# Optimization experiments

Measured on AMD Instinct MI355X. Metric: run time of the kernel, lower is better.

The kernel has to match this reference:

```python
import jax, jax.numpy as jnp
import numpy as np

N, G, H1, H2, HEADS, EMB, C, S = 4096, 2048, 512, 128, 8, 16, 20, 4
CH = H1 // HEADS  # per-head channels = 64
EPS = 1e-6
COEF_FE = 0.1


def _uni(k, shape, fan_in, fan_out):
    c = np.sqrt(6.0 / (fan_in + fan_out)).astype(np.float32)
    return jax.random.uniform(k, shape, jnp.float32, -c, c)


def setup_inputs() -> dict:
    key = jax.random.key(0)
    ks = jax.random.split(key, 40)
    adj = (jax.random.uniform(ks[0], (N, N)) < 0.005).astype(jnp.float32)
    adj = jnp.maximum(adj, jnp.eye(N, dtype=jnp.float32))  # self-loops, no empty rows
    node_feats = jax.random.normal(ks[1], (N, G), jnp.float32)
    count_matrix = jax.random.randint(ks[2], (N, G), 0, 50).astype(jnp.float32)
    library_size = jax.random.uniform(ks[3], (N, 1), jnp.float32, 0.5, 2.0)
    slice_label = jax.random.randint(ks[4], (N,), 0, S)
    basis = jax.random.uniform(ks[5], (C, G), jnp.float32)
    # encoder GAT layer1: HEADS heads, c_in=G -> c_out=CH each
    We1 = _uni(ks[6], (HEADS, CH, G), G, CH)
    be1 = jnp.zeros((HEADS, CH), jnp.float32)
    v0e1 = _uni(ks[7], (HEADS, CH, 1), CH, 1)
    v1e1 = _uni(ks[8], (HEADS, CH, 1), CH, 1)
    # encoder dense layer2: H1 -> H2
    W2 = _uni(ks[9], (H2, H1), H1, H2)
    b2 = jnp.zeros((H2,), jnp.float32)
    # decoder GAT layer1: c_in = H2+EMB -> CH per head
    CIN_D = H2 + EMB
    Wd1 = _uni(ks[10], (HEADS, CH, CIN_D), CIN_D, CH)
    bd1 = jnp.zeros((HEADS, CH), jnp.float32)
    v0d1 = _uni(ks[11], (HEADS, CH, 1), CH, 1)
    v1d1 = _uni(ks[12], (HEADS, CH, 1), CH, 1)
    # decoder dense layer2: H1 -> G
    Wd2 = _uni(ks[13], (G, H1), H1, G)
    bd2 = jnp.zeros((G,), jnp.float32)
    # deconv alpha (H2+EMB -> 1) and beta (H2 -> C); zero-init in torch, small random here
    Wa = 0.01 * jax.random.normal(ks[14], (1, CIN_D), jnp.float32)
    ba = jnp.zeros((1,), jnp.float32)
    Wb = 0.01 * jax.random.normal(ks[15], (C, H2), jnp.float32)
    bb = jnp.zeros((C,), jnp.float32)
    gamma = 0.01 * jax.random.normal(ks[16], (S, G), jnp.float32)
    logtheta = 5.0 * jnp.ones((S, G), jnp.float32)
    emb_table = jax.random.normal(ks[17], (S, EMB), jnp.float32)
    return dict(adj_matrix=adj, node_feats=node_feats, count_matrix=count_matrix,
                library_size=library_size, slice_label=slice_label, basis=basis,
                We1=We1, be1=be1, v0e1=v0e1, v1e1=v1e1, W2=W2, b2=b2,
                Wd1=Wd1, bd1=bd1, v0d1=v0d1, v1d1=v1d1, Wd2=Wd2, bd2=bd2,
                Wa=Wa, ba=ba, Wb=Wb, bb=bb, gamma=gamma, logtheta=logtheta,
                emb_table=emb_table)


def _gat_head(x, adj, W, b, v0, v1):
    h = x @ W.T + b                       # [N, CH]
    logits = adj * ((h @ v0) + (h @ v1).T)  # [N, N]; zero where adj==0
    s = jax.nn.sigmoid(logits) - 0.5       # unnormalized attentions
    mask = adj != 0.0
    e = jnp.where(mask, jnp.exp(s), 0.0)    # sparse softmax over structural nonzeros (temp=1)
    den = e.sum(axis=1, keepdims=True)
    p = e / jnp.where(den == 0.0, 1.0, den)
    return p @ h                            # [N, CH]


def _gat_multi(x, adj, Ws, bs, v0s, v1s):
    return jnp.concatenate([_gat_head(x, adj, Ws[i], bs[i], v0s[i], v1s[i])
                            for i in range(HEADS)], axis=1)


def reference(adj_matrix, node_feats, count_matrix, library_size, slice_label, basis,
              We1, be1, v0e1, v1e1, W2, b2, Wd1, bd1, v0d1, v1d1, Wd2, bd2,
              Wa, ba, Wb, bb, gamma, logtheta, emb_table):
    # encoder
    H = jax.nn.elu(_gat_multi(node_feats, adj_matrix, We1, be1, v0e1, v1e1))
    Z = H @ W2.T + b2                                   # [N, H2]
    emb = emb_table[slice_label]                        # [N, EMB]
    # deconvolutioner
    beta = jax.nn.softmax(jax.nn.elu(Z) @ Wb.T + bb, axis=1)   # [N, C]
    Hc = jax.nn.elu(jnp.concatenate([Z, emb], axis=1))
    alpha = Hc @ Wa.T + ba                              # [N, 1]
    # decoder
    Hd = jax.nn.elu(_gat_multi(jnp.concatenate([Z, emb], axis=1), adj_matrix,
                               Wd1, bd1, v0d1, v1d1))
    X_recon = Hd @ Wd2.T + bd2                          # [N, G]
    features_loss = jnp.mean(jnp.sqrt(jnp.sum((node_feats - X_recon) ** 2, axis=1)))
    # NB deconvolution loss
    log_lam = jnp.log(beta @ basis + EPS) + alpha + gamma[slice_label]
    lam = jnp.exp(log_lam)
    th = jnp.exp(logtheta)[slice_label]                 # [N, G]
    mu = library_size * lam
    ll = (jax.lax.lgamma(count_matrix + th + EPS) - jax.lax.lgamma(th + EPS)
          + th * jnp.log(th + EPS) - th * jnp.log(th + mu + EPS)
          + count_matrix * jnp.log(mu + EPS) - count_matrix * jnp.log(th + mu + EPS))
    decon_loss = -jnp.mean(jnp.sum(ll, axis=1))
    return decon_loss + COEF_FE * features_loss
```

## Files before the change

### kernel.cpp

```cpp
#include <hip/hip_runtime.h>
#include <hip/hip_bf16.h>
#include <math.h>

#define N 4096
#define G 2048
#define H1 512
#define H2 128
#define HEADS 8
#define EMB 16
#define C 20
#define S 4
#define CH 64
#define CIN_D (H2 + EMB)
#define KD_PAD 160
#define KB_PAD 32
#define CAP 128
#define EPSV 1e-6f

typedef __attribute__((ext_vector_type(8))) short short8;
typedef __attribute__((ext_vector_type(8))) short bf16x8;
typedef __attribute__((ext_vector_type(4))) float f32x4;

__device__ __forceinline__ unsigned short f2b(float x) {
    __hip_bfloat16 h = __float2bfloat16(x);
    return *reinterpret_cast<unsigned short*>(&h);
}
__device__ __forceinline__ float b2f(unsigned short u) {
    unsigned int x = ((unsigned int)u) << 16;
    return __uint_as_float(x);
}
__device__ __forceinline__ float lgamma_fast(float x) {
    float sh = 0.f;
    while (x < 8.f) { sh -= __logf(x); x += 1.f; }
    float ix = 1.f / x;
    float lx = __logf(x);
    return (x - 0.5f) * lx - x + 0.91893853f
         + ix * (0.08333333f - 0.00277778f * ix * ix) + sh;
}

__global__ void build_csr(const float* __restrict__ adj, int* __restrict__ col_idx,
                          int* __restrict__ row_cnt) {
    int i = blockIdx.x;
    int lane = threadIdx.x;
    int cnt = 0;
    const float4* row4 = (const float4*)(adj + (size_t)i * N);
    int* cols = col_idx + (size_t)i * CAP;
    unsigned long long lmask = (1ull << lane) - 1ull;
    for (int c = 0; c < N / 256; ++c) {
        float4 v = row4[c * 64 + lane];
        float vv[4] = {v.x, v.y, v.z, v.w};
        #pragma unroll
        for (int s = 0; s < 4; ++s) {
            unsigned long long m = __ballot(vv[s] != 0.f);
            if (vv[s] != 0.f) {
                int idx = cnt + __popcll(m & lmask);
                if (idx < CAP) cols[idx] = c * 256 + lane * 4 + s;
            }
            cnt += __popcll(m);
        }
    }
    if (lane == 0) row_cnt[i] = cnt < CAP ? cnt : CAP;
}

#define SEG_SG   (S * G)
#define SEG_NF4  (N * G / 4)
#define SEG_WE4  (H1 * G / 4)
#define SEG_W24  (H2 * H1 / 4)
#define SEG_WD1E (H1 * KD_PAD)
#define SEG_WD24 (G * H1 / 4)
#define SEG_BTE  (G * KB_PAD)
#define PREP_TOTAL (SEG_SG + SEG_NF4 + SEG_WE4 + SEG_W24 + SEG_WD1E + SEG_WD24 + SEG_BTE)

__device__ __forceinline__ void cvt4(const float* __restrict__ in,
                                     unsigned short* __restrict__ out, int i) {
    float4 v = ((const float4*)in)[i];
    ushort4 o;
    o.x = f2b(v.x); o.y = f2b(v.y); o.z = f2b(v.z); o.w = f2b(v.w);
    ((ushort4*)out)[i] = o;
}

__global__ __launch_bounds__(256) void prep(const float* __restrict__ logtheta,
                                            const float* __restrict__ gamma,
                                            float* __restrict__ th_a, float* __restrict__ eg_a,
                                            float* __restrict__ gm_a, float* __restrict__ ax_a,
                                            const float* __restrict__ node_f,
                                            unsigned short* __restrict__ nf_bf,
                                            const float* __restrict__ We1,
                                            unsigned short* __restrict__ We1_bf,
                                            const float* __restrict__ W2,
                                            unsigned short* __restrict__ W2_bf,
                                            const float* __restrict__ Wd1,
                                            unsigned short* __restrict__ Wd1_bf,
                                            const float* __restrict__ Wd2,
                                            unsigned short* __restrict__ Wd2_bf,
                                            const float* __restrict__ basis,
                                            unsigned short* __restrict__ basisT_bf) {
    int idx = blockIdx.x * 256 + threadIdx.x;
    if (idx < SEG_SG) {
        float th = __expf(logtheta[idx]);
        float gm = gamma[idx];
        th_a[idx] = th;
        eg_a[idx] = __expf(gm);
        gm_a[idx] = gm;
        ax_a[idx] = th * __logf(th + EPSV) - lgammaf(th + EPSV);
        return;
    }
    idx -= SEG_SG;
    if (idx < SEG_NF4) { cvt4(node_f, nf_bf, idx); return; }
    idx -= SEG_NF4;
    if (idx < SEG_WE4) { cvt4(We1, We1_bf, idx); return; }
    idx -= SEG_WE4;
    if (idx < SEG_W24) { cvt4(W2, W2_bf, idx); return; }
    idx -= SEG_W24;
    if (idx < SEG_WD1E) {
        int n = idx / KD_PAD, k = idx - n * KD_PAD;
        Wd1_bf[idx] = f2b(k < CIN_D ? Wd1[n * CIN_D + k] : 0.f);
        return;
    }
    idx -= SEG_WD1E;
    if (idx < SEG_WD24) { cvt4(Wd2, Wd2_bf, idx); return; }
    idx -= SEG_WD24;
    if (idx < SEG_BTE) {
        int g = idx >> 5, c = idx & 31;
        basisT_bf[idx] = f2b(c < C ? basis[c * G + g] : 0.f);
    }
}

#define LDP 40
template<int FM, int OBF, int KS>
__global__ __launch_bounds__(256) void gemm_mfma(const unsigned short* __restrict__ A,
                                                 const unsigned short* __restrict__ B,
                                                 const float* __restrict__ bias,
                                                 void* __restrict__ Cout,
                                                 int M, int Nc, int K) {
    constexpr int BMT = FM * 32;
    __shared__ short As[BMT * LDP];
    __shared__ short Bs[128 * LDP];
    int bn = blockIdx.x, bm = blockIdx.y;
    int kz = (KS > 1) ? blockIdx.z : 0;
    int t = threadIdx.x;
    int lane = t & 63, wid = t >> 6;
    int wr = wid >> 1, wc = wid & 1;
    f32x4 acc[FM][4] = {};
    const short* Ag = (const short*)A + (size_t)(bm * BMT) * K;
    const short* Bg = (const short*)B + (size_t)(bn * 128) * K;
    int r0 = t >> 2, q0 = t & 3;
    int rbase = (lane & 15);
    int koff = (lane >> 4) * 8;
    int kbeg = kz * (K / KS), kend = kbeg + K / KS;

    for (int k0 = kbeg; k0 < kend; k0 += 32) {
        short8 a0 = *(const short8*)(Ag + (size_t)r0 * K + k0 + q0 * 8);
        short8 a1;
        if constexpr (FM == 4) a1 = *(const short8*)(Ag + (size_t)(r0 + 64) * K + k0 + q0 * 8);
        short8 b0 = *(const short8*)(Bg + (size_t)r0 * K + k0 + q0 * 8);
        short8 b1 = *(const short8*)(Bg + (size_t)(r0 + 64) * K + k0 + q0 * 8);
        __syncthreads();
        *(short8*)(As + r0 * LDP + q0 * 8) = a0;
        if constexpr (FM == 4) *(short8*)(As + (r0 + 64) * LDP + q0 * 8) = a1;
        *(short8*)(Bs + r0 * LDP + q0 * 8) = b0;
        *(short8*)(Bs + (r0 + 64) * LDP + q0 * 8) = b1;
        __syncthreads();
        bf16x8 af[FM], bfr[4];
        #pragma unroll
        for (int m = 0; m < FM; ++m)
            af[m] = *(const bf16x8*)(As + (wr * FM * 16 + m * 16 + rbase) * LDP + koff);
        #pragma unroll
        for (int n = 0; n < 4; ++n)
            bfr[n] = *(const bf16x8*)(Bs + (wc * 64 + n * 16 + rbase) * LDP + koff);
        #pragma unroll
        for (int m = 0; m < FM; ++m)
            #pragma unroll
            for (int n = 0; n < 4; ++n)
                acc[m][n] = __builtin_amdgcn_mfma_f32_16x16x32_bf16(af[m], bfr[n], acc[m][n], 0, 0, 0);
    }
    int colb = bn * 128 + wc * 64;
    int rowb = bm * BMT + wr * FM * 16;
    #pragma unroll
    for (int m = 0; m < FM; ++m) {
        #pragma unroll
        for (int n = 0; n < 4; ++n) {
            int col = colb + n * 16 + (lane & 15);
            int row0 = rowb + m * 16 + (lane >> 4) * 4;
            if constexpr (KS > 1) {
                float* Cp = (float*)Cout + (size_t)kz * M * Nc;
                #pragma unroll
                for (int r = 0; r < 4; ++r)
                    Cp[(size_t)(row0 + r) * Nc + col] = acc[m][n][r];
            } else {
                float bs = bias ? bias[col] : 0.f;
                #pragma unroll
                for (int r = 0; r < 4; ++r) {
                    float v = acc[m][n][r] + bs;
                    if constexpr (OBF)
                        ((unsigned short*)Cout)[(size_t)(row0 + r) * Nc + col] = f2b(v);
                    else
                        ((float*)Cout)[(size_t)(row0 + r) * Nc + col] = v;
                }
            }
        }
    }
}

template<int KS, int OBF>
__global__ __launch_bounds__(256) void reduce_k(const float* __restrict__ Cp,
                                                const float* __restrict__ bias,
                                                void* __restrict__ out,
                                                int total4, int ncmask) {
    int i = blockIdx.x * 256 + threadIdx.x;
    if (i >= total4) return;
    float4 s = ((const float4*)Cp)[i];
    #pragma unroll
    for (int ks = 1; ks < KS; ++ks) {
        float4 v = ((const float4*)(Cp + (size_t)ks * total4 * 4))[i];
        s.x += v.x; s.y += v.y; s.z += v.z; s.w += v.w;
    }
    int col = (i * 4) & ncmask;
    s.x += bias[col]; s.y += bias[col + 1]; s.z += bias[col + 2]; s.w += bias[col + 3];
    if constexpr (OBF) {
        ushort4 o;
        o.x = f2b(s.x); o.y = f2b(s.y); o.z = f2b(s.z); o.w = f2b(s.w);
        ((ushort4*)out)[i] = o;
    } else {
        ((float4*)out)[i] = s;
    }
}

__global__ __launch_bounds__(256) void gemm_recon_sq(const unsigned short* __restrict__ A,
                                                     const unsigned short* __restrict__ B,
                                                     const float* __restrict__ bias,
                                                     const unsigned short* __restrict__ nfb,
                                                     float* __restrict__ sq_part) {
    constexpr int K = H1;
    __shared__ short As[64 * LDP];
    __shared__ short Bs[128 * LDP];
    __shared__ float red[4][32];
    int bn = blockIdx.x, bm = blockIdx.y;
    int t = threadIdx.x;
    int lane = t & 63, wid = t >> 6;
    int wr = wid >> 1, wc = wid & 1;
    f32x4 acc[2][4] = {};
    const short* Ag = (const short*)A + (size_t)(bm * 64) * K;
    const short* Bg = (const short*)B + (size_t)(bn * 128) * K;
    int r0 = t >> 2, q0 = t & 3;
    int rbase = (lane & 15);
    int koff = (lane >> 4) * 8;

    for (int k0 = 0; k0 < K; k0 += 32) {
        short8 a0 = *(const short8*)(Ag + (size_t)r0 * K + k0 + q0 * 8);
        short8 b0 = *(const short8*)(Bg + (size_t)r0 * K + k0 + q0 * 8);
        short8 b1 = *(const short8*)(Bg + (size_t)(r0 + 64) * K + k0 + q0 * 8);
        __syncthreads();
        *(short8*)(As + r0 * LDP + q0 * 8) = a0;
        *(short8*)(Bs + r0 * LDP + q0 * 8) = b0;
        *(short8*)(Bs + (r0 + 64) * LDP + q0 * 8) = b1;
        __syncthreads();
        bf16x8 af[2], bfr[4];
        #pragma unroll
        for (int m = 0; m < 2; ++m)
            af[m] = *(const bf16x8*)(As + (wr * 32 + m * 16 + rbase) * LDP + koff);
        #pragma unroll
        for (int n = 0; n < 4; ++n)
            bfr[n] = *(const bf16x8*)(Bs + (wc * 64 + n * 16 + rbase) * LDP + koff);
        #pragma unroll
        for (int m = 0; m < 2; ++m)
            #pragma unroll
            for (int n = 0; n < 4; ++n)
                acc[m][n] = __builtin_amdgcn_mfma_f32_16x16x32_bf16(af[m], bfr[n], acc[m][n], 0, 0, 0);
    }
    int colb = bn * 128 + wc * 64;
    int rowb = bm * 64 + wr * 32;
    float part[2][4];
    #pragma unroll
    for (int m = 0; m < 2; ++m) {
        #pragma unroll
        for (int r = 0; r < 4; ++r) part[m][r] = 0.f;
        #pragma unroll
        for (int n = 0; n < 4; ++n) {
            int col = colb + n * 16 + (lane & 15);
            float bs = bias[col];
            int row0 = rowb + m * 16 + (lane >> 4) * 4;
            #pragma unroll
            for (int r = 0; r < 4; ++r) {
                float d = b2f(nfb[(size_t)(row0 + r) * G + col]) - (acc[m][n][r] + bs);
                part[m][r] += d * d;
            }
        }
    }
    #pragma unroll
    for (int m = 0; m < 2; ++m)
        #pragma unroll
        for (int r = 0; r < 4; ++r) {
            float v = part[m][r];
            v += __shfl_xor(v, 1); v += __shfl_xor(v, 2);
            v += __shfl_xor(v, 4); v += __shfl_xor(v, 8);
            part[m][r] = v;
        }
    if ((lane & 15) == 0) {
        int q = lane >> 4;
        #pragma unroll
        for (int m = 0; m < 2; ++m)
            #pragma unroll
            for (int r = 0; r < 4; ++r)
                red[wid][m * 16 + q * 4 + r] = part[m][r];
    }
    __syncthreads();
    if (t < 64) {
        int wr2 = t >> 5, loc = t & 31;
        float v = red[wr2 * 2 + 0][loc] + red[wr2 * 2 + 1][loc];
        sq_part[(size_t)(bm * 64 + t) * 16 + bn] = v;
    }
}

__global__ __launch_bounds__(256) void nb_loss_ew(const unsigned short* __restrict__ BDb,
                                                  const float* __restrict__ cm,
                                                  const int* __restrict__ slab,
                                                  const float* __restrict__ muf,
                                                  const float* __restrict__ kco,
                                                  const float* __restrict__ th_a,
                                                  const float* __restrict__ eg_a,
                                                  const float* __restrict__ gm_a,
                                                  const float* __restrict__ ax_a,
                                                  float* __restrict__ ll_row) {
    int row = blockIdx.x * 4 + (threadIdx.x >> 6);
    int lane = threadIdx.x & 63;
    int sl = slab[row];
    float mufv = muf[row], kcov = kco[row];
    const unsigned short* bdr = BDb + (size_t)row * G;
    const float* cmr = cm + (size_t)row * G;
    size_t sgb = (size_t)sl * G;
    float acc = 0.f;
    #pragma unroll 2
    for (int it = 0; it < G / 256; ++it) {
        int c = it * 256 + lane * 4;
        ushort4 bdu = *(const ushort4*)(bdr + c);
        f32x4 k4  = *(const f32x4*)(cmr + c);
        f32x4 th4 = *(const f32x4*)(th_a + sgb + c);
        f32x4 eg4 = *(const f32x4*)(eg_a + sgb + c);
        f32x4 gm4 = *(const f32x4*)(gm_a + sgb + c);
        f32x4 ax4 = *(const f32x4*)(ax_a + sgb + c);
        float bdv[4] = {b2f(bdu.x), b2f(bdu.y), b2f(bdu.z), b2f(bdu.w)};
        #pragma unroll
        for (int j = 0; j < 4; ++j) {
            float th = th4[j], k = k4[j];
            float ebd = bdv[j] + EPSV;
            float lbd = __logf(ebd);
            float mu = mufv * ebd * eg4[j];
            float lgx = lgamma_fast(k + th + EPSV);
            acc += lgx + ax4[j] - (th + k) * __logf(th + mu + EPSV)
                 + k * (kcov + lbd + gm4[j]);
        }
    }
    #pragma unroll
    for (int m = 32; m; m >>= 1) acc += __shfl_xor(acc, m);
    if (lane == 0) ll_row[row] = acc;
}

__global__ void head_dots(const unsigned short* __restrict__ Hb, const float* __restrict__ v0,
                          const float* __restrict__ v1, float* __restrict__ hv0,
                          float* __restrict__ hv1) {
    int i = blockIdx.x;
    int lane = threadIdx.x;
    #pragma unroll
    for (int h = 0; h < HEADS; ++h) {
        float v = b2f(Hb[(size_t)i * H1 + h * CH + lane]);
        float p0 = v * v0[h * CH + lane];
        float p1 = v * v1[h * CH + lane];
        #pragma unroll
        for (int m = 32; m; m >>= 1) {
            p0 += __shfl_xor(p0, m);
            p1 += __shfl_xor(p1, m);
        }
        if (lane == 0) {
            hv0[i * HEADS + h] = p0;
            hv1[i * HEADS + h] = p1;
        }
    }
}

__global__ __launch_bounds__(512) void attn_fused(const unsigned short* __restrict__ Hb,
                                                  const float* __restrict__ hv0,
                                                  const float* __restrict__ hv1,
                                                  const int* __restrict__ col_idx,
                                                  const int* __restrict__ row_cnt,
                                                  unsigned short* __restrict__ out) {
    __shared__ int scols[CAP];
    __shared__ float sw[CAP][HEADS];
    __shared__ float sden[HEADS];
    __shared__ float red[8][64 * 8];
    int i = blockIdx.x;
    int t = threadIdx.x;
    int cnt = row_cnt[i];
    const int* cols = col_idx + (size_t)i * CAP;
    if (t < cnt) scols[t] = cols[t];
    __syncthreads();
    for (int idx = t; idx < cnt * HEADS; idx += 512) {
        int e = idx >> 3, h = idx & 7;
        int j = scols[e];
        float x = hv0[i * HEADS + h] + hv1[j * HEADS + h];
        sw[e][h] = __expf(1.f / (1.f + __expf(-x)) - 0.5f);
    }
    __syncthreads();
    if (t < HEADS) {
        float d = 0.f;
        for (int e = 0; e < cnt; ++e) d += sw[e][t];
        sden[t] = 1.f / d;
    }
    __syncthreads();
    int slot = t >> 6;
    int cg = t & 63;
    int h = cg >> 3;
    float inv = sden[h];
    float acc[8];
    #pragma unroll
    for (int k = 0; k < 8; ++k) acc[k] = 0.f;
    for (int e = slot; e < cnt; e += 8) {
        int j = scols[e];
        float wv = sw[e][h] * inv;
        short8 hv = ((const short8*)(Hb + (size_t)j * H1))[cg];
        #pragma unroll
        for (int k = 0; k < 8; ++k)
            acc[k] += wv * b2f((unsigned short)hv[k]);
    }
    #pragma unroll
    for (int k = 0; k < 8; ++k) red[slot][cg * 8 + k] = acc[k];
    __syncthreads();
    if (slot < 4) {
        #pragma unroll
        for (int k = 0; k < 8; ++k) red[slot][cg * 8 + k] += red[slot + 4][cg * 8 + k];
    }
    __syncthreads();
    if (slot < 2) {
        #pragma unroll
        for (int k = 0; k < 8; ++k) red[slot][cg * 8 + k] += red[slot + 2][cg * 8 + k];
    }
    __syncthreads();
    if (slot == 0) {
        short8 o;
        #pragma unroll
        for (int k = 0; k < 8; ++k) {
            float v = red[0][cg * 8 + k] + red[1][cg * 8 + k];
            v = (v > 0.f) ? v : expm1f(v);
            o[k] = (short)f2b(v);
        }
        ((short8*)(out + (size_t)i * H1))[cg] = o;
    }
}

__global__ void pernode(const float* __restrict__ Z, const float* __restrict__ emb_table,
                        const int* __restrict__ slab, const float* __restrict__ Wb,
                        const float* __restrict__ bb, const float* __restrict__ Wa,
                        const float* __restrict__ ba, const float* __restrict__ lib,
                        unsigned short* __restrict__ beta_bf, float* __restrict__ muf,
                        float* __restrict__ kco, unsigned short* __restrict__ Xdb) {
    int i = blockIdx.x;
    int lane = threadIdx.x;
    __shared__ float sZ[H2];
    __shared__ float sE[EMB];
    __shared__ float sLog[C];
    __shared__ float sAl;
    sZ[lane] = Z[(size_t)i * H2 + lane];
    sZ[64 + lane] = Z[(size_t)i * H2 + 64 + lane];
    int s = slab[i];
    if (lane < EMB) sE[lane] = emb_table[s * EMB + lane];
    __syncthreads();
    Xdb[(size_t)i * KD_PAD + lane] = f2b(sZ[lane]);
    Xdb[(size_t)i * KD_PAD + 64 + lane] = f2b(sZ[64 + lane]);
    if (lane < EMB) Xdb[(size_t)i * KD_PAD + H2 + lane] = f2b(sE[lane]);
    if (lane < KD_PAD - CIN_D) Xdb[(size_t)i * KD_PAD + CIN_D + lane] = 0;
    if (lane < C) {
        float acc = bb[lane];
        for (int k = 0; k < H2; ++k) {
            float z = sZ[k];
            float e = z > 0.f ? z : expm1f(z);
            acc += e * Wb[lane * H2 + k];
        }
        sLog[lane] = acc;
    }
    __syncthreads();
    if (lane == 0) {
        float mx = sLog[0];
        for (int c = 1; c < C; ++c) mx = fmaxf(mx, sLog[c]);
        float sm = 0.f;
        for (int c = 0; c < C; ++c) { float e = __expf(sLog[c] - mx); sLog[c] = e; sm += e; }
        for (int c = 0; c < C; ++c) sLog[c] /= sm;
    }
    __syncthreads();
    if (lane < KB_PAD) beta_bf[(size_t)i * KB_PAD + lane] = (lane < C) ? f2b(sLog[lane]) : 0;
    float x0 = sZ[lane];        x0 = x0 > 0.f ? x0 : expm1f(x0);
    float x1 = sZ[64 + lane];   x1 = x1 > 0.f ? x1 : expm1f(x1);
    float p = x0 * Wa[lane] + x1 * Wa[64 + lane];
    if (lane < EMB) {
        float x2 = sE[lane];    x2 = x2 > 0.f ? x2 : expm1f(x2);
        p += x2 * Wa[H2 + lane];
    }
    #pragma unroll
    for (int m = 32; m; m >>= 1) p += __shfl_xor(p, m);
    if (lane == 0) sAl = p + ba[0];
    __syncthreads();
    if (lane == 0) {
        float A = sAl, L = lib[i];
        muf[i] = L * __expf(A);
        kco[i] = __logf(L) + A;
    }
}

__global__ void row_reduce(const float* __restrict__ ll_row, const float* __restrict__ sq_part,
                           float* __restrict__ part_ll, float* __restrict__ part_sq) {
    int blk = blockIdx.x, lane = threadIdx.x;
    int row = blk * 64 + lane;
    float s1 = ll_row[row];
    float s2 = 0.f;
    #pragma unroll
    for (int j = 0; j < 16; ++j) s2 += sq_part[(size_t)row * 16 + j];
    float b = sqrtf(s2);
    #pragma unroll
    for (int m = 32; m; m >>= 1) { s1 += __shfl_xor(s1, m); b += __shfl_xor(b, m); }
    if (lane == 0) { part_ll[blk] = s1; part_sq[blk] = b; }
}

__global__ void finalize2(const float* __restrict__ part_ll, const float* __restrict__ part_sq,
                          float* __restrict__ out) {
    int lane = threadIdx.x;
    float a = part_ll[lane], b = part_sq[lane];
    #pragma unroll
    for (int m = 32; m; m >>= 1) { a += __shfl_xor(a, m); b += __shfl_xor(b, m); }
    if (lane == 0) out[0] = -(a / (float)N) + 0.1f * (b / (float)N);
}

extern "C" void kernel_launch(void* const* d_in, const int* in_sizes, int n_in,
                              void* d_out, int out_size, void* d_ws, size_t ws_size,
                              hipStream_t stream) {
    const float* adj       = (const float*)d_in[0];
    const float* node_f    = (const float*)d_in[1];
    const float* count_m   = (const float*)d_in[2];
    const float* lib       = (const float*)d_in[3];
    const int*   slab      = (const int*)d_in[4];
    const float* basis     = (const float*)d_in[5];
    const float* We1       = (const float*)d_in[6];
    const float* be1       = (const float*)d_in[7];
    const float* v0e1      = (const float*)d_in[8];
    const float* v1e1      = (const float*)d_in[9];
    const float* W2        = (const float*)d_in[10];
    const float* b2        = (const float*)d_in[11];
    const float* Wd1       = (const float*)d_in[12];
    const float* bd1       = (const float*)d_in[13];
    const float* v0d1      = (const float*)d_in[14];
    const float* v1d1      = (const float*)d_in[15];
    const float* Wd2       = (const float*)d_in[16];
    const float* bd2       = (const float*)d_in[17];
    const float* Wa        = (const float*)d_in[18];
    const float* ba        = (const float*)d_in[19];
    const float* Wb        = (const float*)d_in[20];
    const float* bb        = (const float*)d_in[21];
    const float* gamma     = (const float*)d_in[22];
    const float* logtheta  = (const float*)d_in[23];
    const float* emb_table = (const float*)d_in[24];
    float* out = (float*)d_out;

    char* w = (char*)d_ws;
    auto alloc = [&](size_t bytes) { void* p = (void*)w; w += (bytes + 255) & ~(size_t)255; return p; };
    int*   col_idx = (int*)  alloc((size_t)N * CAP * 4);
    int*   row_cnt = (int*)  alloc((size_t)N * 4);
    unsigned short* Hlin_bf = (unsigned short*)alloc((size_t)N * H1 * 2);
    unsigned short* Hgat_bf = (unsigned short*)alloc((size_t)N * H1 * 2);
    float* Z       = (float*)alloc((size_t)N * H2 * 4);
    unsigned short* Xd_bf   = (unsigned short*)alloc((size_t)N * KD_PAD * 2);
    unsigned short* beta_bf = (unsigned short*)alloc((size_t)N * KB_PAD * 2);
    float* muf     = (float*)alloc((size_t)N * 4);
    float* kco     = (float*)alloc((size_t)N * 4);
    float* hv0     = (float*)alloc((size_t)N * HEADS * 4);
    float* hv1     = (float*)alloc((size_t)N * HEADS * 4);
    float* th_a    = (float*)alloc((size_t)S * G * 4);
    float* eg_a    = (float*)alloc((size_t)S * G * 4);
    float* gm_a    = (float*)alloc((size_t)S * G * 4);
    float* ax_a    = (float*)alloc((size_t)S * G * 4);
    float* Cp      = (float*)alloc((size_t)4 * N * H1 * 4);
    unsigned short* BDb = (unsigned short*)alloc((size_t)N * G * 2);
    float* ll_row  = (float*)alloc((size_t)N * 4);
    float* sq_part = (float*)alloc((size_t)N * 16 * 4);
    float* part_ll = (float*)alloc(64 * 4);
    float* part_sq = (float*)alloc(64 * 4);
    unsigned short* nf_bf    = (unsigned short*)alloc((size_t)N * G * 2);
    unsigned short* We1_bf   = (unsigned short*)alloc((size_t)H1 * G * 2);
    unsigned short* W2_bf    = (unsigned short*)alloc((size_t)H2 * H1 * 2);
    unsigned short* Wd1_bf   = (unsigned short*)alloc((size_t)H1 * KD_PAD * 2);
    unsigned short* Wd2_bf   = (unsigned short*)alloc((size_t)G * H1 * 2);
    unsigned short* basisT_bf= (unsigned short*)alloc((size_t)G * KB_PAD * 2);

    build_csr<<<dim3(N), dim3(64), 0, stream>>>(adj, col_idx, row_cnt);
    prep<<<dim3(PREP_TOTAL / 256), dim3(256), 0, stream>>>(
        logtheta, gamma, th_a, eg_a, gm_a, ax_a,
        node_f, nf_bf, We1, We1_bf, W2, W2_bf, Wd1, Wd1_bf, Wd2, Wd2_bf, basis, basisT_bf);

    gemm_mfma<2, 0, 4><<<dim3(H1 / 128, N / 64, 4), dim3(256), 0, stream>>>(
        nf_bf, We1_bf, be1, Cp, N, H1, G);
    reduce_k<4, 1><<<dim3((N * H1 / 4 + 255) / 256), dim3(256), 0, stream>>>(
        Cp, be1, Hlin_bf, N * H1 / 4, H1 - 1);
    head_dots<<<dim3(N), dim3(64), 0, stream>>>(Hlin_bf, v0e1, v1e1, hv0, hv1);
    attn_fused<<<dim3(N), dim3(512), 0, stream>>>(Hlin_bf, hv0, hv1, col_idx, row_cnt, Hgat_bf);
    gemm_mfma<2, 0, 8><<<dim3(H2 / 128, N / 64, 8), dim3(256), 0, stream>>>(
        Hgat_bf, W2_bf, b2, Cp, N, H2, H1);
    reduce_k<8, 0><<<dim3((N * H2 / 4 + 255) / 256), dim3(256), 0, stream>>>(
        Cp, b2, Z, N * H2 / 4, H2 - 1);
    pernode<<<dim3(N), dim3(64), 0, stream>>>(Z, emb_table, slab, Wb, bb, Wa, ba, lib,
                                              beta_bf, muf, kco, Xd_bf);
    gemm_mfma<2, 1, 1><<<dim3(G / 128, N / 64), dim3(256), 0, stream>>>(
        beta_bf, basisT_bf, nullptr, BDb, N, G, KB_PAD);
    nb_loss_ew<<<dim3(N / 4), dim3(256), 0, stream>>>(
        BDb, count_m, slab, muf, kco, th_a, eg_a, gm_a, ax_a, ll_row);
    gemm_mfma<2, 1, 1><<<dim3(H1 / 128, N / 64), dim3(256), 0, stream>>>(
        Xd_bf, Wd1_bf, bd1, Hlin_bf, N, H1, KD_PAD);
    head_dots<<<dim3(N), dim3(64), 0, stream>>>(Hlin_bf, v0d1, v1d1, hv0, hv1);
    attn_fused<<<dim3(N), dim3(512), 0, stream>>>(Hlin_bf, hv0, hv1, col_idx, row_cnt, Hgat_bf);
    gemm_recon_sq<<<dim3(G / 128, N / 64), dim3(256), 0, stream>>>(
        Hgat_bf, Wd2_bf, bd2, nf_bf, sq_part);
    row_reduce<<<dim3(64), dim3(64), 0, stream>>>(ll_row, sq_part, part_ll, part_sq);
    finalize2<<<dim3(1), dim3(64), 0, stream>>>(part_ll, part_sq, out);
}
```

Before: 201.7 us.

## Fuse head dot products into GEMM epilogues and NB loss into basis GEMM

Drops the separate head_dots kernels. The attention head dot products are now computed in the split-K reduce epilogue for the encoder and in the GEMM epilogue for the decoder. The beta@basis GEMM is fused with the NB log-likelihood evaluation, so the N×G bf16 intermediate is never written to or read back from global memory; per-tile partial sums are reduced in row_reduce. This removes kernel launches and a large intermediate round trip. In exchange, the fused loss reads count and per-slice arrays with scalar strided accesses instead of vectorized rows, and extra epilogue work may add register pressure.

Measured after the change: 186.1 us. -7.7%, faster.

```diff
diff --git a/kernel.cpp b/kernel.cpp
--- a/kernel.cpp
+++ b/kernel.cpp
@@ -127,12 +127,16 @@
 }
 
 #define LDP 40
-template<int FM, int OBF, int KS>
+template<int FM, int OBF, int KS, int HV>
 __global__ __launch_bounds__(256) void gemm_mfma(const unsigned short* __restrict__ A,
                                                  const unsigned short* __restrict__ B,
                                                  const float* __restrict__ bias,
                                                  void* __restrict__ Cout,
-                                                 int M, int Nc, int K) {
+                                                 int M, int Nc, int K,
+                                                 const float* __restrict__ v0f,
+                                                 const float* __restrict__ v1f,
+                                                 float* __restrict__ hv0,
+                                                 float* __restrict__ hv1) {
     constexpr int BMT = FM * 32;
     __shared__ short As[BMT * LDP];
     __shared__ short Bs[128 * LDP];
@@ -200,12 +204,38 @@
             }
         }
     }
-}
-
-template<int KS, int OBF>
+    if constexpr (HV) {
+        int h = colb >> 6;
+        #pragma unroll
+        for (int m = 0; m < FM; ++m) {
+            #pragma unroll
+            for (int r = 0; r < 4; ++r) {
+                int row = rowb + m * 16 + (lane >> 4) * 4 + r;
+                float p0 = 0.f, p1 = 0.f;
+                #pragma unroll
+                for (int n = 0; n < 4; ++n) {
+                    int col = colb + n * 16 + (lane & 15);
+                    float v = acc[m][n][r] + bias[col];
+                    p0 += v * v0f[col];
+                    p1 += v * v1f[col];
+                }
+                p0 += __shfl_xor(p0, 1); p0 += __shfl_xor(p0, 2);
+                p0 += __shfl_xor(p0, 4); p0 += __shfl_xor(p0, 8);
+                p1 += __shfl_xor(p1, 1); p1 += __shfl_xor(p1, 2);
+                p1 += __shfl_xor(p1, 4); p1 += __shfl_xor(p1, 8);
+                if ((lane & 15) == 0) {
+                    hv0[row * HEADS + h] = p0;
+                    hv1[row * HEADS + h] = p1;
+                }
+            }
+        }
+    }
+}
+
+template<int KS>
 __global__ __launch_bounds__(256) void reduce_k(const float* __restrict__ Cp,
                                                 const float* __restrict__ bias,
-                                                void* __restrict__ out,
+                                                float* __restrict__ out,
                                                 int total4, int ncmask) {
     int i = blockIdx.x * 256 + threadIdx.x;
     if (i >= total4) return;
@@ -217,12 +247,44 @@
     }
     int col = (i * 4) & ncmask;
     s.x += bias[col]; s.y += bias[col + 1]; s.z += bias[col + 2]; s.w += bias[col + 3];
-    if constexpr (OBF) {
-        ushort4 o;
-        o.x = f2b(s.x); o.y = f2b(s.y); o.z = f2b(s.z); o.w = f2b(s.w);
-        ((ushort4*)out)[i] = o;
-    } else {
-        ((float4*)out)[i] = s;
+    ((float4*)out)[i] = s;
+}
+
+template<int KS>
+__global__ __launch_bounds__(256) void reduce_k_hv(const float* __restrict__ Cp,
+                                                   const float* __restrict__ bias,
+                                                   unsigned short* __restrict__ out,
+                                                   const float* __restrict__ v0f,
+                                                   const float* __restrict__ v1f,
+                                                   float* __restrict__ hv0,
+                                                   float* __restrict__ hv1) {
+    constexpr int total4 = N * H1 / 4;
+    int t = threadIdx.x;
+    int i = blockIdx.x * 256 + t;
+    float4 s = ((const float4*)Cp)[i];
+    #pragma unroll
+    for (int ks = 1; ks < KS; ++ks) {
+        float4 v = ((const float4*)(Cp + (size_t)ks * total4 * 4))[i];
+        s.x += v.x; s.y += v.y; s.z += v.z; s.w += v.w;
+    }
+    int col = (i * 4) & (H1 - 1);
+    s.x += bias[col]; s.y += bias[col + 1]; s.z += bias[col + 2]; s.w += bias[col + 3];
+    ushort4 o;
+    o.x = f2b(s.x); o.y = f2b(s.y); o.z = f2b(s.z); o.w = f2b(s.w);
+    ((ushort4*)out)[i] = o;
+    int row = (i * 4) >> 9;
+    int h = col >> 6;
+    float4 w0 = *(const float4*)(v0f + col);
+    float4 w1 = *(const float4*)(v1f + col);
+    float p0 = s.x * w0.x + s.y * w0.y + s.z * w0.z + s.w * w0.w;
+    float p1 = s.x * w1.x + s.y * w1.y + s.z * w1.z + s.w * w1.w;
+    p0 += __shfl_xor(p0, 1); p0 += __shfl_xor(p0, 2);
+    p0 += __shfl_xor(p0, 4); p0 += __shfl_xor(p0, 8);
+    p1 += __shfl_xor(p1, 1); p1 += __shfl_xor(p1, 2);
+    p1 += __shfl_xor(p1, 4); p1 += __shfl_xor(p1, 8);
+    if ((t & 15) == 0) {
+        hv0[row * HEADS + h] = p0;
+        hv1[row * HEADS + h] = p1;
     }
 }
 
@@ -312,69 +374,79 @@
     }
 }
 
-__global__ __launch_bounds__(256) void nb_loss_ew(const unsigned short* __restrict__ BDb,
-                                                  const float* __restrict__ cm,
-                                                  const int* __restrict__ slab,
-                                                  const float* __restrict__ muf,
-                                                  const float* __restrict__ kco,
-                                                  const float* __restrict__ th_a,
-                                                  const float* __restrict__ eg_a,
-                                                  const float* __restrict__ gm_a,
-                                                  const float* __restrict__ ax_a,
-                                                  float* __restrict__ ll_row) {
-    int row = blockIdx.x * 4 + (threadIdx.x >> 6);
-    int lane = threadIdx.x & 63;
-    int sl = slab[row];
-    float mufv = muf[row], kcov = kco[row];
-    const unsigned short* bdr = BDb + (size_t)row * G;
-    const float* cmr = cm + (size_t)row * G;
-    size_t sgb = (size_t)sl * G;
-    float acc = 0.f;
-    #pragma unroll 2
-    for (int it = 0; it < G / 256; ++it) {
-        int c = it * 256 + lane * 4;
-        ushort4 bdu = *(const ushort4*)(bdr + c);
-        f32x4 k4  = *(const f32x4*)(cmr + c);
-        f32x4 th4 = *(const f32x4*)(th_a + sgb + c);
-        f32x4 eg4 = *(const f32x4*)(eg_a + sgb + c);
-        f32x4 gm4 = *(const f32x4*)(gm_a + sgb + c);
-        f32x4 ax4 = *(const f32x4*)(ax_a + sgb + c);
-        float bdv[4] = {b2f(bdu.x), b2f(bdu.y), b2f(bdu.z), b2f(bdu.w)};
-        #pragma unroll
-        for (int j = 0; j < 4; ++j) {
-            float th = th4[j], k = k4[j];
-            float ebd = bdv[j] + EPSV;
+__global__ __launch_bounds__(256) void bd_ll(const unsigned short* __restrict__ A,
+                                             const unsigned short* __restrict__ B,
+                                             const float* __restrict__ cm,
+                                             const int* __restrict__ slab,
+                                             const float* __restrict__ muf,
+                                             const float* __restrict__ kco,
+                                             const float* __restrict__ th_a,
+                                             const float* __restrict__ eg_a,
+                                             const float* __restrict__ gm_a,
+                                             const float* __restrict__ ax_a,
+                                             float* __restrict__ ll_part) {
+    __shared__ short As[32 * LDP];
+    __shared__ short Bs[128 * LDP];
+    __shared__ float red[4][16];
+    int bn = blockIdx.x, bm = blockIdx.y;
+    int t = threadIdx.x;
+    int lane = t & 63, wid = t >> 6;
+    int wr = wid >> 1, wc = wid & 1;
+    f32x4 acc[4] = {};
+    const short* Ag = (const short*)A + (size_t)(bm * 32) * KB_PAD;
+    const short* Bg = (const short*)B + (size_t)(bn * 128) * KB_PAD;
+    int r0 = t >> 2, q0 = t & 3;
+    if (t < 128) {
+        short8 a0 = *(const short8*)(Ag + (size_t)r0 * KB_PAD + q0 * 8);
+        *(short8*)(As + r0 * LDP + q0 * 8) = a0;
+    }
+    {
+        short8 b0 = *(const short8*)(Bg + (size_t)r0 * KB_PAD + q0 * 8);
+        short8 b1 = *(const short8*)(Bg + (size_t)(r0 + 64) * KB_PAD + q0 * 8);
+        *(short8*)(Bs + r0 * LDP + q0 * 8) = b0;
+        *(short8*)(Bs + (r0 + 64) * LDP + q0 * 8) = b1;
+    }
+    __syncthreads();
+    int rbase = (lane & 15);
+    int koff = (lane >> 4) * 8;
+    bf16x8 af = *(const bf16x8*)(As + (wr * 16 + rbase) * LDP + koff);
+    bf16x8 bfr[4];
+    #pragma unroll
+    for (int n = 0; n < 4; ++n)
+        bfr[n] = *(const bf16x8*)(Bs + (wc * 64 + n * 16 + rbase) * LDP + koff);
+    #pragma unroll
+    for (int n = 0; n < 4; ++n)
+        acc[n] = __builtin_amdgcn_mfma_f32_16x16x32_bf16(af, bfr[n], acc[n], 0, 0, 0);
+    int colb = bn * 128 + wc * 64;
+    int rowb = bm * 32 + wr * 16;
+    #pragma unroll
+    for (int r = 0; r < 4; ++r) {
+        int row = rowb + (lane >> 4) * 4 + r;
+        int sl = slab[row];
+        float mufv = muf[row], kcov = kco[row];
+        size_t sgb = (size_t)sl * G;
+        float p = 0.f;
+        #pragma unroll
+        for (int n = 0; n < 4; ++n) {
+            int col = colb + n * 16 + (lane & 15);
+            float ebd = acc[n][r] + EPSV;
+            float k = cm[(size_t)row * G + col];
+            float th = th_a[sgb + col];
             float lbd = __logf(ebd);
-            float mu = mufv * ebd * eg4[j];
+            float mu = mufv * ebd * eg_a[sgb + col];
             float lgx = lgamma_fast(k + th + EPSV);
-            acc += lgx + ax4[j] - (th + k) * __logf(th + mu + EPSV)
-                 + k * (kcov + lbd + gm4[j]);
-        }
-    }
-    #pragma unroll
-    for (int m = 32; m; m >>= 1) acc += __shfl_xor(acc, m);
-    if (lane == 0) ll_row[row] = acc;
-}
-
-__global__ void head_dots(const unsigned short* __restrict__ Hb, const float* __restrict__ v0,
-                          const float* __restrict__ v1, float* __restrict__ hv0,
-                          float* __restrict__ hv1) {
-    int i = blockIdx.x;
-    int lane = threadIdx.x;
-    #pragma unroll
-    for (int h = 0; h < HEADS; ++h) {
-        float v = b2f(Hb[(size_t)i * H1 + h * CH + lane]);
-        float p0 = v * v0[h * CH + lane];
-        float p1 = v * v1[h * CH + lane];
-        #pragma unroll
-        for (int m = 32; m; m >>= 1) {
-            p0 += __shfl_xor(p0, m);
-            p1 += __shfl_xor(p1, m);
-        }
-        if (lane == 0) {
-            hv0[i * HEADS + h] = p0;
-            hv1[i * HEADS + h] = p1;
-        }
+            p += lgx + ax_a[sgb + col] - (th + k) * __logf(th + mu + EPSV)
+               + k * (kcov + lbd + gm_a[sgb + col]);
+        }
+        p += __shfl_xor(p, 1); p += __shfl_xor(p, 2);
+        p += __shfl_xor(p, 4); p += __shfl_xor(p, 8);
+        if ((lane & 15) == 0) red[wid][(lane >> 4) * 4 + r] = p;
+    }
+    __syncthreads();
+    if (t < 32) {
+        int wr2 = t >> 4, rl = t & 15;
+        float v = red[wr2 * 2 + 0][rl] + red[wr2 * 2 + 1][rl];
+        ll_part[(size_t)(bm * 32 + wr2 * 16 + rl) * 16 + bn] = v;
     }
 }
 
@@ -505,14 +577,16 @@
     }
 }
 
-__global__ void row_reduce(const float* __restrict__ ll_row, const float* __restrict__ sq_part,
+__global__ void row_reduce(const float* __restrict__ ll_part, const float* __restrict__ sq_part,
                            float* __restrict__ part_ll, float* __restrict__ part_sq) {
     int blk = blockIdx.x, lane = threadIdx.x;
     int row = blk * 64 + lane;
-    float s1 = ll_row[row];
-    float s2 = 0.f;
-    #pragma unroll
-    for (int j = 0; j < 16; ++j) s2 += sq_part[(size_t)row * 16 + j];
+    float s1 = 0.f, s2 = 0.f;
+    #pragma unroll
+    for (int j = 0; j < 16; ++j) {
+        s1 += ll_part[(size_t)row * 16 + j];
+        s2 += sq_part[(size_t)row * 16 + j];
+    }
     float b = sqrtf(s2);
     #pragma unroll
     for (int m = 32; m; m >>= 1) { s1 += __shfl_xor(s1, m); b += __shfl_xor(b, m); }
@@ -576,8 +650,7 @@
     float* gm_a    = (float*)alloc((size_t)S * G * 4);
     float* ax_a    = (float*)alloc((size_t)S * G * 4);
     float* Cp      = (float*)alloc((size_t)4 * N * H1 * 4);
-    unsigned short* BDb = (unsigned short*)alloc((size_t)N * G * 2);
-    float* ll_row  = (float*)alloc((size_t)N * 4);
+    float* ll_part = (float*)alloc((size_t)N * 16 * 4);
     float* sq_part = (float*)alloc((size_t)N * 16 * 4);
     float* part_ll = (float*)alloc(64 * 4);
     float* part_sq = (float*)alloc(64 * 4);
@@ -593,28 +666,24 @@
         logtheta, gamma, th_a, eg_a, gm_a, ax_a,
         node_f, nf_bf, We1, We1_bf, W2, W2_bf, Wd1, Wd1_bf, Wd2, Wd2_bf, basis, basisT_bf);
 
-    gemm_mfma<2, 0, 4><<<dim3(H1 / 128, N / 64, 4), dim3(256), 0, stream>>>(
-        nf_bf, We1_bf, be1, Cp, N, H1, G);
-    reduce_k<4, 1><<<dim3((N * H1 / 4 + 255) / 256), dim3(256), 0, stream>>>(
-        Cp, be1, Hlin_bf, N * H1 / 4, H1 - 1);
-    head_dots<<<dim3(N), dim3(64), 0, stream>>>(Hlin_bf, v0e1, v1e1, hv0, hv1);
+    gemm_mfma<2, 0, 4, 0><<<dim3(H1 / 128, N / 64, 4), dim3(256), 0, stream>>>(
+        nf_bf, We1_bf, be1, Cp, N, H1, G, nullptr, nullptr, nullptr, nullptr);
+    reduce_k_hv<4><<<dim3(N * H1 / 4 / 256), dim3(256), 0, stream>>>(
+        Cp, be1, Hlin_bf, v0e1, v1e1, hv0, hv1);
     attn_fused<<<dim3(N), dim3(512), 0, stream>>>(Hlin_bf, hv0, hv1, col_idx, row_cnt, Hgat_bf);
-    gemm_mfma<2, 0, 8><<<dim3(H2 / 128, N / 64, 8), dim3(256), 0, stream>>>(
-        Hgat_bf, W2_bf, b2, Cp, N, H2, H1);
-    reduce_k<8, 0><<<dim3((N * H2 / 4 + 255) / 256), dim3(256), 0, stream>>>(
+    gemm_mfma<2, 0, 8, 0><<<dim3(H2 / 128, N / 64, 8), dim3(256), 0, stream>>>(
+        Hgat_bf, W2_bf, b2, Cp, N, H2, H1, nullptr, nullptr, nullptr, nullptr);
+    reduce_k<8><<<dim3((N * H2 / 4 + 255) / 256), dim3(256), 0, stream>>>(
         Cp, b2, Z, N * H2 / 4, H2 - 1);
     pernode<<<dim3(N), dim3(64), 0, stream>>>(Z, emb_table, slab, Wb, bb, Wa, ba, lib,
                                               beta_bf, muf, kco, Xd_bf);
-    gemm_mfma<2, 1, 1><<<dim3(G / 128, N / 64), dim3(256), 0, stream>>>(
-        beta_bf, basisT_bf, nullptr, BDb, N, G, KB_PAD);
-    nb_loss_ew<<<dim3(N / 4), dim3(256), 0, stream>>>(
-        BDb, count_m, slab, muf, kco, th_a, eg_a, gm_a, ax_a, ll_row);
-    gemm_mfma<2, 1, 1><<<dim3(H1 / 128, N / 64), dim3(256), 0, stream>>>(
-        Xd_bf, Wd1_bf, bd1, Hlin_bf, N, H1, KD_PAD);
-    head_dots<<<dim3(N), dim3(64), 0, stream>>>(Hlin_bf, v0d1, v1d1, hv0, hv1);
+    bd_ll<<<dim3(G / 128, N / 32), dim3(256), 0, stream>>>(
+        beta_bf, basisT_bf, count_m, slab, muf, kco, th_a, eg_a, gm_a, ax_a, ll_part);
+    gemm_mfma<2, 1, 1, 1><<<dim3(H1 / 128, N / 64), dim3(256), 0, stream>>>(
+        Xd_bf, Wd1_bf, bd1, Hlin_bf, N, H1, KD_PAD, v0d1, v1d1, hv0, hv1);
     attn_fused<<<dim3(N), dim3(512), 0, stream>>>(Hlin_bf, hv0, hv1, col_idx, row_cnt, Hgat_bf);
     gemm_recon_sq<<<dim3(G / 128, N / 64), dim3(256), 0, stream>>>(
         Hgat_bf, Wd2_bf, bd2, nf_bf, sq_part);
-    row_reduce<<<dim3(64), dim3(64), 0, stream>>>(ll_row, sq_part, part_ll, part_sq);
+    row_reduce<<<dim3(64), dim3(64), 0, stream>>>(ll_part, sq_part, part_ll, part_sq);
     finalize2<<<dim3(1), dim3(64), 0, stream>>>(part_ll, part_sq, out);
 }
```
